# Kernel optimization log

Hardware: AMD Instinct MI355X
Metric: run time of the kernel (lower is better)

The kernel has to match this reference:

```python
import jax, jax.numpy as jnp
import numpy as np

B, C, P, H, W = 32, 256, 8, 64, 64
BN_EPS = 1e-5


def setup_inputs() -> dict:
    key = jax.random.key(0)
    ks = jax.random.split(key, 8)
    x = jax.random.normal(ks[0], (B, C, H, W), dtype=jnp.float32)
    # 1x1 conv C->C stored as (C_out, C_in)
    W1 = jax.random.normal(ks[1], (C, C), dtype=jnp.float32) * (1.0 / np.sqrt(C))
    b1 = jax.random.normal(ks[2], (C,), dtype=jnp.float32) * 0.01
    gamma = jnp.ones((C,), dtype=jnp.float32)
    beta = jnp.zeros((C,), dtype=jnp.float32)
    mean = jax.random.normal(ks[3], (C,), dtype=jnp.float32) * 0.01
    var = jnp.abs(jax.random.normal(ks[4], (C,), dtype=jnp.float32)) + 1.0
    # 1x1 conv C->P
    W2 = jax.random.normal(ks[5], (P, C), dtype=jnp.float32) * (1.0 / np.sqrt(C))
    b2 = jax.random.normal(ks[6], (P,), dtype=jnp.float32) * 0.01
    return {"x": x, "W1": W1, "b1": b1, "gamma": gamma, "beta": beta,
            "mean": mean, "var": var, "W2": W2, "b2": b2}


def reference(x, W1, b1, gamma, beta, mean, var, W2, b2):
    # conv1x1 (C->C) + BatchNorm (inference, running stats) + ReLU
    h = jnp.einsum('oc,bchw->bohw', W1, x) + b1[None, :, None, None]
    inv = gamma * jax.lax.rsqrt(var + BN_EPS)            # (C,)
    h = h * inv[None, :, None, None] + (beta - mean * inv)[None, :, None, None]
    h = jax.nn.relu(h)
    # conv1x1 (C->P) + sigmoid -> soft part masks (B,P,H,W)
    mask = jax.nn.sigmoid(jnp.einsum('pc,bchw->bphw', W2, h) + b2[None, :, None, None])
    # feature_map2vec fused as a batched matmul over HW (avoids (B,C,P,HW) blowup)
    sum_w = jnp.sum(mask, axis=(-1, -2)) + 1e-12          # (B,P)
    vec = jnp.einsum('bchw,bphw->bcp', x, mask)           # (B,C,P)
    vec = vec / sum_w[:, None, :]
    # torch: view(B, C*P) then reshape(B, P, -1) -> raw row-major reshape, NOT a transpose
    return vec.reshape(B, P, C)
```

## Files before the change

kernel.cpp:

```cpp
#include <hip/hip_runtime.h>

typedef _Float16 f16;
typedef f16 f16x8 __attribute__((ext_vector_type(8)));
typedef f16 f16x4 __attribute__((ext_vector_type(4)));
typedef float f32x4 __attribute__((ext_vector_type(4)));

#define NB 32
#define NC 256
#define NP 8
#define NHW 4096

#define AH_OFF 0u
#define AL_OFF 131072u
#define CV_OFF 262144u
#define PV_OFF 263168u
#define PS_OFF 4457472u

#define XS_PITCH 528
#define XS_LO    33792
#define DP_OFF   67584
#define MLS_OFF  75776
#define SMEM_BYTES 79872

#define SWZ(s) ((((s) >> 2) & 7) << 4)

#define MFMA16(a, b, c) __builtin_amdgcn_mfma_f32_16x16x32_f16(a, b, c, 0, 0, 0)

__global__ __launch_bounds__(256) void k_prep(
    const float* __restrict__ W1, const float* __restrict__ b1,
    const float* __restrict__ gamma, const float* __restrict__ beta,
    const float* __restrict__ mean, const float* __restrict__ var,
    f16* __restrict__ Ah, f16* __restrict__ Al, float* __restrict__ cvec) {
  const int o = blockIdx.x;
  const int k = threadIdx.x;
  const float inv = gamma[o] * rsqrtf(var[o] + 1e-5f);
  const float a = W1[o * NC + k] * inv;
  const f16 hi = (f16)a;
  Ah[o * NC + k] = hi;
  Al[o * NC + k] = (f16)((a - (float)hi) * 512.0f);
  if (k == 0) cvec[o] = (b1[o] - mean[o]) * inv + beta[o];
}

__global__ __launch_bounds__(256)
__attribute__((amdgpu_waves_per_eu(2, 2)))
void k_fused(
    const float* __restrict__ x, const f16* __restrict__ Ah,
    const f16* __restrict__ Al, const float* __restrict__ cvec,
    const float* __restrict__ W2, const float* __restrict__ b2,
    float* __restrict__ pvec_t, float* __restrict__ psw_t) {
  extern __shared__ __align__(16) char sm[];
  const int b  = blockIdx.x >> 4;
  const int tg = blockIdx.x & 15;
  const int t  = threadIdx.x;
  const int w    = t >> 6;
  const int lane = t & 63;
  const int lg = lane >> 4;
  const int ln = lane & 15;
  const int cb = t >> 2;
  const int sq = t & 3;

  float accv[4][8];
  float smac[8];
  #pragma unroll
  for (int j = 0; j < 4; ++j)
    #pragma unroll
    for (int p = 0; p < 8; ++p) accv[j][p] = 0.f;
  #pragma unroll
  for (int p = 0; p < 8; ++p) smac[p] = 0.f;

  for (int tt = 0; tt < 4; ++tt) {
    const int hw0 = (tg * 4 + tt) * 64;
    __syncthreads();

    {
      const float* xb = x + (size_t)b * NC * NHW + hw0;
      #pragma unroll
      for (int i = 0; i < 4; ++i) {
        const int id = i * 256 + t;
        const int cbs = id >> 4;
        const int sb  = id & 15;
        const float* r0 = xb + (size_t)(cbs * 4) * NHW + sb * 4;
        const float4 v0 = *(const float4*)(r0);
        const float4 v1 = *(const float4*)(r0 + NHW);
        const float4 v2 = *(const float4*)(r0 + 2 * NHW);
        const float4 v3 = *(const float4*)(r0 + 3 * NHW);
        #pragma unroll
        for (int j = 0; j < 4; ++j) {
          const float e0 = ((const float*)&v0)[j];
          const float e1 = ((const float*)&v1)[j];
          const float e2 = ((const float*)&v2)[j];
          const float e3 = ((const float*)&v3)[j];
          const f16 h0 = (f16)e0, h1 = (f16)e1, h2 = (f16)e2, h3 = (f16)e3;
          const f16 l0 = (f16)((e0 - (float)h0) * 512.0f);
          const f16 l1 = (f16)((e1 - (float)h1) * 512.0f);
          const f16 l2 = (f16)((e2 - (float)h2) * 512.0f);
          const f16 l3 = (f16)((e3 - (float)h3) * 512.0f);
          const int s = sb * 4 + j;
          char* dst = sm + s * XS_PITCH + ((cbs * 8) ^ SWZ(s));
          *(f16x4*)dst = (f16x4){h0, h1, h2, h3};
          *(f16x4*)(dst + XS_LO) = (f16x4){l0, l1, l2, l3};
        }
      }
    }
    __syncthreads();

    f32x4 acc1[4][4] = {};
    f32x4 acc2[4][4] = {};
    #pragma unroll 1
    for (int k0 = 0; k0 < 8; ++k0) {
      f16x8 ah[4], xh[4], xo[4];
      #pragma unroll
      for (int mi = 0; mi < 4; ++mi) {
        const size_t off = (size_t)((w * 64 + mi * 16 + ln) * NC + k0 * 32 + lg * 8);
        ah[mi] = *(const f16x8*)(Ah + off);
      }
      #pragma unroll
      for (int nf = 0; nf < 4; ++nf) {
        const int s = nf * 16 + ln;
        xh[nf] = *(const f16x8*)(sm + s * XS_PITCH + ((k0 * 64 + lg * 16) ^ SWZ(s)));
      }
      #pragma unroll
      for (int mi = 0; mi < 4; ++mi)
        #pragma unroll
        for (int nf = 0; nf < 4; ++nf)
          acc1[mi][nf] = MFMA16(ah[mi], xh[nf], acc1[mi][nf]);

      #pragma unroll
      for (int nf = 0; nf < 4; ++nf) {
        const int s = nf * 16 + ln;
        xo[nf] = *(const f16x8*)(sm + XS_LO + s * XS_PITCH + ((k0 * 64 + lg * 16) ^ SWZ(s)));
      }
      #pragma unroll
      for (int mi = 0; mi < 4; ++mi)
        #pragma unroll
        for (int nf = 0; nf < 4; ++nf)
          acc2[mi][nf] = MFMA16(ah[mi], xo[nf], acc2[mi][nf]);

      #pragma unroll
      for (int mi = 0; mi < 4; ++mi) {
        const size_t off = (size_t)((w * 64 + mi * 16 + ln) * NC + k0 * 32 + lg * 8);
        xo[mi] = *(const f16x8*)(Al + off);
      }
      #pragma unroll
      for (int mi = 0; mi < 4; ++mi)
        #pragma unroll
        for (int nf = 0; nf < 4; ++nf)
          acc2[mi][nf] = MFMA16(xo[mi], xh[nf], acc2[mi][nf]);
    }

    {
      f32x4 cv[4];
      #pragma unroll
      for (int mi = 0; mi < 4; ++mi)
        cv[mi] = *(const f32x4*)(cvec + w * 64 + mi * 16 + lg * 4);
      #pragma unroll
      for (int mi = 0; mi < 4; ++mi)
        #pragma unroll
        for (int nf = 0; nf < 4; ++nf)
          #pragma unroll
          for (int r = 0; r < 4; ++r) {
            const float v = acc1[mi][nf][r] + acc2[mi][nf][r] * (1.0f / 512.0f) + cv[mi][r];
            acc1[mi][nf][r] = v > 0.0f ? v : 0.0f;
          }

      float pd[8][4] = {};
      #pragma unroll
      for (int p = 0; p < 8; ++p)
        #pragma unroll
        for (int mi = 0; mi < 4; ++mi) {
          const f32x4 w4 = *(const f32x4*)(W2 + p * NC + w * 64 + mi * 16 + lg * 4);
          #pragma unroll
          for (int nf = 0; nf < 4; ++nf)
            pd[p][nf] += w4[0] * acc1[mi][nf][0] + w4[1] * acc1[mi][nf][1]
                       + w4[2] * acc1[mi][nf][2] + w4[3] * acc1[mi][nf][3];
        }
      #pragma unroll
      for (int p = 0; p < 8; ++p)
        #pragma unroll
        for (int nf = 0; nf < 4; ++nf) {
          pd[p][nf] += __shfl_xor(pd[p][nf], 16, 64);
          pd[p][nf] += __shfl_xor(pd[p][nf], 32, 64);
        }
      float* dpart = (float*)(sm + DP_OFF);
      if (lg == 0) {
        #pragma unroll
        for (int p = 0; p < 8; ++p)
          #pragma unroll
          for (int nf = 0; nf < 4; ++nf)
            dpart[w * 512 + p * 64 + nf * 16 + ln] = pd[p][nf];
      }
    }
    __syncthreads();

    {
      const float* dp = (const float*)(sm + DP_OFF);
      float* mls = (float*)(sm + MLS_OFF);
      #pragma unroll
      for (int it = 0; it < 2; ++it) {
        const int id = it * 256 + t;
        const int p = id >> 6, s = id & 63;
        float d = b2[p];
        #pragma unroll
        for (int ww = 0; ww < 4; ++ww) d += dp[ww * 512 + p * 64 + s];
        const float m = 1.0f / (1.0f + __expf(-d));
        mls[s * 16 + ((s >> 4) & 1) * 4 + p] = m;
      }
    }
    __syncthreads();

    {
      const float* mlsr = (const float*)(sm + MLS_OFF);
      #pragma unroll 4
      for (int i = 0; i < 16; ++i) {
        const int s = sq * 16 + i;
        const float* mrow = mlsr + s * 16 + ((s >> 4) & 1) * 4;
        const f32x4 m0 = *(const f32x4*)mrow;
        const f32x4 m1 = *(const f32x4*)(mrow + 4);
        const char* xrow = sm + s * XS_PITCH + ((cb * 8) ^ SWZ(s));
        const f16x4 h4 = *(const f16x4*)xrow;
        const f16x4 l4 = *(const f16x4*)(xrow + XS_LO);
        #pragma unroll
        for (int j = 0; j < 4; ++j) {
          const float xf = (float)h4[j] + (float)l4[j] * (1.0f / 512.0f);
          #pragma unroll
          for (int p = 0; p < 4; ++p) {
            accv[j][p]     += xf * m0[p];
            accv[j][p + 4] += xf * m1[p];
          }
        }
        #pragma unroll
        for (int p = 0; p < 4; ++p) { smac[p] += m0[p]; smac[p + 4] += m1[p]; }
      }
    }
  }

  #pragma unroll
  for (int j = 0; j < 4; ++j)
    #pragma unroll
    for (int p = 0; p < 8; ++p) {
      accv[j][p] += __shfl_xor(accv[j][p], 1, 64);
      accv[j][p] += __shfl_xor(accv[j][p], 2, 64);
    }
  #pragma unroll
  for (int p = 0; p < 8; ++p) {
    smac[p] += __shfl_xor(smac[p], 1, 64);
    smac[p] += __shfl_xor(smac[p], 2, 64);
  }

  f32x4 o0, o1;
  #pragma unroll
  for (int p = 0; p < 8; ++p) {
    const float v01 = (sq & 1) ? accv[1][p] : accv[0][p];
    const float v23 = (sq & 1) ? accv[3][p] : accv[2][p];
    const float v = (sq & 2) ? v23 : v01;
    if (p < 4) o0[p] = v; else o1[p - 4] = v;
  }
  float* dst = pvec_t + (((size_t)(b * 16 + tg) * 256) + t) * 8;
  *(f32x4*)dst = o0;
  *(f32x4*)(dst + 4) = o1;
  if (t == 0) {
    f32x4 s0, s1;
    #pragma unroll
    for (int p = 0; p < 4; ++p) { s0[p] = smac[p]; s1[p] = smac[p + 4]; }
    float* d2 = psw_t + (size_t)(b * 16 + tg) * 8;
    *(f32x4*)d2 = s0;
    *(f32x4*)(d2 + 4) = s1;
  }
}

__global__ __launch_bounds__(256) void k_reduce(
    const float* __restrict__ pvec, const float* __restrict__ psw,
    float* __restrict__ out) {
  const int idx = blockIdx.x * 256 + threadIdx.x;
  const int b = idx >> 11;
  const int cp = idx & 2047;
  const int p = idx & 7;
  float v = 0.f, sw = 1e-12f;
  #pragma unroll
  for (int ch = 0; ch < 16; ++ch) {
    v += pvec[((size_t)(b * 16 + ch)) * 2048 + cp];
    sw += psw[((size_t)(b * 16 + ch)) * 8 + p];
  }
  out[idx] = v / sw;
}

extern "C" void kernel_launch(void* const* d_in, const int* in_sizes, int n_in,
                              void* d_out, int out_size, void* d_ws, size_t ws_size,
                              hipStream_t stream) {
  const float* x     = (const float*)d_in[0];
  const float* W1    = (const float*)d_in[1];
  const float* b1    = (const float*)d_in[2];
  const float* gamma = (const float*)d_in[3];
  const float* beta  = (const float*)d_in[4];
  const float* mean  = (const float*)d_in[5];
  const float* var   = (const float*)d_in[6];
  const float* W2    = (const float*)d_in[7];
  const float* b2    = (const float*)d_in[8];

  char* ws = (char*)d_ws;
  f16* Ah      = (f16*)(ws + AH_OFF);
  f16* Al      = (f16*)(ws + AL_OFF);
  float* cvec  = (float*)(ws + CV_OFF);
  float* pvec_t = (float*)(ws + PV_OFF);
  float* psw_t  = (float*)(ws + PS_OFF);
  float* out   = (float*)d_out;

  (void)hipFuncSetAttribute((const void*)k_fused,
                            hipFuncAttributeMaxDynamicSharedMemorySize,
                            SMEM_BYTES);

  k_prep<<<256, 256, 0, stream>>>(W1, b1, gamma, beta, mean, var, Ah, Al, cvec);
  k_fused<<<512, 256, SMEM_BYTES, stream>>>(x, Ah, Al, cvec, W2, b2, pvec_t, psw_t);
  k_reduce<<<256, 256, 0, stream>>>(pvec_t, psw_t, out);
}
```

Before: 355.0 us.

## Merge split-precision GEMM accumulators and shrink live registers for higher occupancy

The two accumulator sets (hi and correction terms) become a single accumulator. The low-order products are accumulated first, scaled by 1/512, and then the hi*hi product runs in a second k-loop. The per-tile pvec accumulation is moved out of registers and into a global read-modify-write each tile, and the forced waves_per_eu(2,2) attribute is removed. Together these cut register pressure so more waves can be resident. The cost is a second pass over Ah and shared memory, plus extra global traffic for the partial vectors.

Measured after the change: 358.6 us. About the same (+1.0%).

```diff
diff --git a/kernel.cpp b/kernel.cpp
--- a/kernel.cpp
+++ b/kernel.cpp
@@ -41,9 +41,7 @@
   if (k == 0) cvec[o] = (b1[o] - mean[o]) * inv + beta[o];
 }
 
-__global__ __launch_bounds__(256)
-__attribute__((amdgpu_waves_per_eu(2, 2)))
-void k_fused(
+__global__ __launch_bounds__(256) void k_fused(
     const float* __restrict__ x, const f16* __restrict__ Ah,
     const f16* __restrict__ Al, const float* __restrict__ cvec,
     const float* __restrict__ W2, const float* __restrict__ b2,
@@ -59,12 +57,7 @@
   const int cb = t >> 2;
   const int sq = t & 3;
 
-  float accv[4][8];
   float smac[8];
-  #pragma unroll
-  for (int j = 0; j < 4; ++j)
-    #pragma unroll
-    for (int p = 0; p < 8; ++p) accv[j][p] = 0.f;
   #pragma unroll
   for (int p = 0; p < 8; ++p) smac[p] = 0.f;
 
@@ -104,48 +97,59 @@
     }
     __syncthreads();
 
-    f32x4 acc1[4][4] = {};
-    f32x4 acc2[4][4] = {};
+    f32x4 acc[4][4] = {};
     #pragma unroll 1
     for (int k0 = 0; k0 < 8; ++k0) {
-      f16x8 ah[4], xh[4], xo[4];
-      #pragma unroll
-      for (int mi = 0; mi < 4; ++mi) {
-        const size_t off = (size_t)((w * 64 + mi * 16 + ln) * NC + k0 * 32 + lg * 8);
-        ah[mi] = *(const f16x8*)(Ah + off);
-      }
+      f16x8 fa[4], fb[4];
+      #pragma unroll
+      for (int mi = 0; mi < 4; ++mi)
+        fa[mi] = *(const f16x8*)(Ah + (size_t)((w * 64 + mi * 16 + ln) * NC + k0 * 32 + lg * 8));
       #pragma unroll
       for (int nf = 0; nf < 4; ++nf) {
         const int s = nf * 16 + ln;
-        xh[nf] = *(const f16x8*)(sm + s * XS_PITCH + ((k0 * 64 + lg * 16) ^ SWZ(s)));
+        fb[nf] = *(const f16x8*)(sm + XS_LO + s * XS_PITCH + ((k0 * 64 + lg * 16) ^ SWZ(s)));
       }
       #pragma unroll
       for (int mi = 0; mi < 4; ++mi)
         #pragma unroll
         for (int nf = 0; nf < 4; ++nf)
-          acc1[mi][nf] = MFMA16(ah[mi], xh[nf], acc1[mi][nf]);
-
+          acc[mi][nf] = MFMA16(fa[mi], fb[nf], acc[mi][nf]);
+      #pragma unroll
+      for (int mi = 0; mi < 4; ++mi)
+        fa[mi] = *(const f16x8*)(Al + (size_t)((w * 64 + mi * 16 + ln) * NC + k0 * 32 + lg * 8));
       #pragma unroll
       for (int nf = 0; nf < 4; ++nf) {
         const int s = nf * 16 + ln;
-        xo[nf] = *(const f16x8*)(sm + XS_LO + s * XS_PITCH + ((k0 * 64 + lg * 16) ^ SWZ(s)));
+        fb[nf] = *(const f16x8*)(sm + s * XS_PITCH + ((k0 * 64 + lg * 16) ^ SWZ(s)));
       }
       #pragma unroll
       for (int mi = 0; mi < 4; ++mi)
         #pragma unroll
         for (int nf = 0; nf < 4; ++nf)
-          acc2[mi][nf] = MFMA16(ah[mi], xo[nf], acc2[mi][nf]);
-
-      #pragma unroll
-      for (int mi = 0; mi < 4; ++mi) {
-        const size_t off = (size_t)((w * 64 + mi * 16 + ln) * NC + k0 * 32 + lg * 8);
-        xo[mi] = *(const f16x8*)(Al + off);
+          acc[mi][nf] = MFMA16(fa[mi], fb[nf], acc[mi][nf]);
+    }
+    #pragma unroll
+    for (int mi = 0; mi < 4; ++mi)
+      #pragma unroll
+      for (int nf = 0; nf < 4; ++nf)
+        #pragma unroll
+        for (int r = 0; r < 4; ++r) acc[mi][nf][r] *= (1.0f / 512.0f);
+    #pragma unroll 1
+    for (int k0 = 0; k0 < 8; ++k0) {
+      f16x8 fa[4], fb[4];
+      #pragma unroll
+      for (int mi = 0; mi < 4; ++mi)
+        fa[mi] = *(const f16x8*)(Ah + (size_t)((w * 64 + mi * 16 + ln) * NC + k0 * 32 + lg * 8));
+      #pragma unroll
+      for (int nf = 0; nf < 4; ++nf) {
+        const int s = nf * 16 + ln;
+        fb[nf] = *(const f16x8*)(sm + s * XS_PITCH + ((k0 * 64 + lg * 16) ^ SWZ(s)));
       }
       #pragma unroll
       for (int mi = 0; mi < 4; ++mi)
         #pragma unroll
         for (int nf = 0; nf < 4; ++nf)
-          acc2[mi][nf] = MFMA16(xo[mi], xh[nf], acc2[mi][nf]);
+          acc[mi][nf] = MFMA16(fa[mi], fb[nf], acc[mi][nf]);
     }
 
     {
@@ -159,8 +163,8 @@
         for (int nf = 0; nf < 4; ++nf)
           #pragma unroll
           for (int r = 0; r < 4; ++r) {
-            const float v = acc1[mi][nf][r] + acc2[mi][nf][r] * (1.0f / 512.0f) + cv[mi][r];
-            acc1[mi][nf][r] = v > 0.0f ? v : 0.0f;
+            const float v = acc[mi][nf][r] + cv[mi][r];
+            acc[mi][nf][r] = v > 0.0f ? v : 0.0f;
           }
 
       float pd[8][4] = {};
@@ -171,8 +175,8 @@
           const f32x4 w4 = *(const f32x4*)(W2 + p * NC + w * 64 + mi * 16 + lg * 4);
           #pragma unroll
           for (int nf = 0; nf < 4; ++nf)
-            pd[p][nf] += w4[0] * acc1[mi][nf][0] + w4[1] * acc1[mi][nf][1]
-                       + w4[2] * acc1[mi][nf][2] + w4[3] * acc1[mi][nf][3];
+            pd[p][nf] += w4[0] * acc[mi][nf][0] + w4[1] * acc[mi][nf][1]
+                       + w4[2] * acc[mi][nf][2] + w4[3] * acc[mi][nf][3];
         }
       #pragma unroll
       for (int p = 0; p < 8; ++p)
@@ -209,6 +213,12 @@
     __syncthreads();
 
     {
+      float accv[4][8];
+      #pragma unroll
+      for (int j = 0; j < 4; ++j)
+        #pragma unroll
+        for (int p = 0; p < 8; ++p) accv[j][p] = 0.f;
+
       const float* mlsr = (const float*)(sm + MLS_OFF);
       #pragma unroll 4
       for (int i = 0; i < 16; ++i) {
@@ -231,33 +241,40 @@
         #pragma unroll
         for (int p = 0; p < 4; ++p) { smac[p] += m0[p]; smac[p + 4] += m1[p]; }
       }
+
+      #pragma unroll
+      for (int j = 0; j < 4; ++j)
+        #pragma unroll
+        for (int p = 0; p < 8; ++p) {
+          accv[j][p] += __shfl_xor(accv[j][p], 1, 64);
+          accv[j][p] += __shfl_xor(accv[j][p], 2, 64);
+        }
+      f32x4 o0, o1;
+      #pragma unroll
+      for (int p = 0; p < 8; ++p) {
+        const float v01 = (sq & 1) ? accv[1][p] : accv[0][p];
+        const float v23 = (sq & 1) ? accv[3][p] : accv[2][p];
+        const float v = (sq & 2) ? v23 : v01;
+        if (p < 4) o0[p] = v; else o1[p - 4] = v;
+      }
+      float* dst = pvec_t + (((size_t)(b * 16 + tg) * 256) + t) * 8;
+      if (tt == 0) {
+        *(f32x4*)dst = o0;
+        *(f32x4*)(dst + 4) = o1;
+      } else {
+        const f32x4 a0 = *(const f32x4*)dst;
+        const f32x4 a1 = *(const f32x4*)(dst + 4);
+        *(f32x4*)dst = o0 + a0;
+        *(f32x4*)(dst + 4) = o1 + a1;
+      }
     }
   }
 
-  #pragma unroll
-  for (int j = 0; j < 4; ++j)
-    #pragma unroll
-    for (int p = 0; p < 8; ++p) {
-      accv[j][p] += __shfl_xor(accv[j][p], 1, 64);
-      accv[j][p] += __shfl_xor(accv[j][p], 2, 64);
-    }
   #pragma unroll
   for (int p = 0; p < 8; ++p) {
     smac[p] += __shfl_xor(smac[p], 1, 64);
     smac[p] += __shfl_xor(smac[p], 2, 64);
   }
-
-  f32x4 o0, o1;
-  #pragma unroll
-  for (int p = 0; p < 8; ++p) {
-    const float v01 = (sq & 1) ? accv[1][p] : accv[0][p];
-    const float v23 = (sq & 1) ? accv[3][p] : accv[2][p];
-    const float v = (sq & 2) ? v23 : v01;
-    if (p < 4) o0[p] = v; else o1[p - 4] = v;
-  }
-  float* dst = pvec_t + (((size_t)(b * 16 + tg) * 256) + t) * 8;
-  *(f32x4*)dst = o0;
-  *(f32x4*)(dst + 4) = o1;
   if (t == 0) {
     f32x4 s0, s1;
     #pragma unroll
```
